# Performance work log

Hardware: AMD Instinct MI355X
Metric: run time of the kernel (lower is better)

The kernel has to match this reference:

```python
import jax, jax.numpy as jnp
import numpy as np


def _mlp(x, w1, b1, w2, b2):
    # full_connected / full_connected_conv1d with channels [3,16,32]:
    # pointwise Linear -> LeakyReLU -> Linear (kernel-size-1 conv == linear on last dim)
    h = jax.nn.leaky_relu(x @ w1 + b1)
    return h @ w2 + b2


def setup_inputs() -> dict:
    key = jax.random.key(0)
    ks = jax.random.split(key, 10)
    P, K = 100000, 16            # points, neighbors per point
    C_IN, C_H, C_OUT, C_W = 3, 16, 32, 64
    center = jax.random.normal(ks[0], (P, 1, C_IN), dtype=jnp.float32)
    other = jax.random.normal(ks[1], (P, K, C_IN), dtype=jnp.float32)
    s1 = 1.0 / np.sqrt(C_IN)
    s2 = 1.0 / np.sqrt(C_H)
    # 6 stacked 3->16->32 MLPs: [q, center_k, center_v, other_k, other_v, pos]
    mlp_w1 = jax.random.normal(ks[2], (6, C_IN, C_H), dtype=jnp.float32) * s1
    mlp_b1 = jax.random.normal(ks[3], (6, C_H), dtype=jnp.float32) * s1
    mlp_w2 = jax.random.normal(ks[4], (6, C_H, C_OUT), dtype=jnp.float32) * s2
    mlp_b2 = jax.random.normal(ks[5], (6, C_OUT), dtype=jnp.float32) * s2
    # weight_process: 32->64->32
    wp_w1 = jax.random.normal(ks[6], (C_OUT, C_W), dtype=jnp.float32) / np.sqrt(C_OUT)
    wp_b1 = jax.random.normal(ks[7], (C_W,), dtype=jnp.float32) / np.sqrt(C_OUT)
    wp_w2 = jax.random.normal(ks[8], (C_W, C_OUT), dtype=jnp.float32) / np.sqrt(C_W)
    wp_b2 = jax.random.normal(ks[9], (C_OUT,), dtype=jnp.float32) / np.sqrt(C_W)
    return {"center": center, "other": other,
            "mlp_w1": mlp_w1, "mlp_b1": mlp_b1, "mlp_w2": mlp_w2, "mlp_b2": mlp_b2,
            "wp_w1": wp_w1, "wp_b1": wp_b1, "wp_w2": wp_w2, "wp_b2": wp_b2}


def reference(center, other, mlp_w1, mlp_b1, mlp_w2, mlp_b2, wp_w1, wp_b1, wp_w2, wp_b2):
    # center: [P,1,3], other: [P,K,3]
    q = _mlp(center, mlp_w1[0], mlp_b1[0], mlp_w2[0], mlp_b2[0])      # [P,1,32]
    ck = _mlp(center, mlp_w1[1], mlp_b1[1], mlp_w2[1], mlp_b2[1])     # [P,1,32]
    cv = _mlp(center, mlp_w1[2], mlp_b1[2], mlp_w2[2], mlp_b2[2])     # [P,1,32]
    ok = _mlp(other, mlp_w1[3], mlp_b1[3], mlp_w2[3], mlp_b2[3])      # [P,K,32]
    ov = _mlp(other, mlp_w1[4], mlp_b1[4], mlp_w2[4], mlp_b2[4])      # [P,K,32]
    k_all = jnp.concatenate([ck, ok], axis=-2)                        # [P,K+1,32]
    v_all = jnp.concatenate([cv, ov], axis=-2)                        # [P,K+1,32]
    fea_minus = center - jnp.concatenate([center, other], axis=-2)    # [P,K+1,3]
    pos = _mlp(fea_minus, mlp_w1[5], mlp_b1[5], mlp_w2[5], mlp_b2[5]) # [P,K+1,32]
    fea_weight = _mlp(q - k_all + pos, wp_w1, wp_b1, wp_w2, wp_b2)    # [P,K+1,32]
    # vector attention: softmax over CHANNEL dim (-1), weighted sum over neighbors (-2)
    attn = jax.nn.softmax(fea_weight, axis=-1) * (v_all + pos)
    return jnp.sum(attn, axis=-2)                                     # [P,32]
```

## Files before the change

### kernel.cpp

```cpp
#include <hip/hip_runtime.h>


constexpr int PPB = 15;
constexpr float LOG2E = 1.44269504088896340736f;

typedef __attribute__((ext_vector_type(8))) short bf8;
typedef __attribute__((ext_vector_type(4))) float f4;

__device__ __forceinline__ float lrelu(float v) { return fmaxf(v, 0.01f * v); }

__device__ __forceinline__ unsigned int pkbf(float a, float b) {
#if __has_builtin(__builtin_amdgcn_cvt_pk_bf16_f32)
  typedef __attribute__((ext_vector_type(2))) __bf16 bf16x2;
  const bf16x2 r = __builtin_amdgcn_cvt_pk_bf16_f32(a, b);
  return __builtin_bit_cast(unsigned int, r);
#else
  const unsigned int ua = __builtin_bit_cast(unsigned int, a) + 0x8000u;
  const unsigned int ub = __builtin_bit_cast(unsigned int, b) + 0x8000u;
  return __builtin_amdgcn_perm(ub, ua, 0x07060302u);
#endif
}
__device__ __forceinline__ unsigned short us16(float a) {
  return (unsigned short)((__builtin_bit_cast(unsigned int, a) + 0x8000u) >> 16);
}
__device__ __forceinline__ bf8 mkbf8(const f4& a, const f4& b) {
  uint4 u;
  u.x = pkbf(a[0], a[1]); u.y = pkbf(a[2], a[3]);
  u.z = pkbf(b[0], b[1]); u.w = pkbf(b[2], b[3]);
  return __builtin_bit_cast(bf8, u);
}
__device__ __forceinline__ float exp2fast(float x) {
#if __has_builtin(__builtin_amdgcn_exp2f)
  return __builtin_amdgcn_exp2f(x);
#else
  float r; asm("v_exp_f32 %0, %1" : "=v"(r) : "v"(x)); return r;
#endif
}
__device__ __forceinline__ f4 mfma32(bf8 a, bf8 b, f4 c) {
  return __builtin_amdgcn_mfma_f32_16x16x32_bf16(a, b, c, 0, 0, 0);
}

__device__ __forceinline__ int slotk(int q, int j) {
  return (j < 4) ? (q * 4 + j) : (16 + q * 4 + (j - 4));
}

__device__ __forceinline__ float w1v(const float* mw1, const float* mb1,
                                     int s, int k, int n) {
  const int cb = n >> 4, cc = n & 15;
  const int sk = s ? 1 : 3, sv = s ? 2 : 4;
  if (k < 3)  return cb == 0 ? mw1[sk * 48 + k * 16 + cc]
                   : (cb == 1 ? mw1[sv * 48 + k * 16 + cc] : 0.f);
  if (k < 6)  return cb == 2 ? mw1[5 * 48 + (k - 3) * 16 + cc] : 0.f;
  if (k < 9)  return cb == 3 ? mw1[0 * 48 + (k - 6) * 16 + cc] : 0.f;
  if (k == 9) {
    const int m = (cb == 0) ? sk : (cb == 1) ? sv : (cb == 2) ? 5 : 0;
    return mb1[m * 16 + cc];
  }
  return 0.f;
}
__device__ __forceinline__ float w2v(const float* mw2, int s, int k, int n) {
  const int sk = s ? 1 : 3, sv = s ? 2 : 4;
  if (n < 32) {
    if (k < 16)            return -mw2[sk * 512 + k * 32 + n];
    if (k >= 32 && k < 48) return  mw2[5 * 512 + (k - 32) * 32 + n];
    if (k >= 48)           return  mw2[0 * 512 + (k - 48) * 32 + n];
    return 0.f;
  } else {
    const int cc = n - 32;
    if (k >= 16 && k < 32) return mw2[sv * 512 + (k - 16) * 32 + cc];
    if (k >= 32 && k < 48) return mw2[5 * 512 + (k - 32) * 32 + cc];
    return 0.f;
  }
}

__global__ void prep_kernel(const float* __restrict__ mw1, const float* __restrict__ mb1,
                            const float* __restrict__ mw2, const float* __restrict__ mb2,
                            const float* __restrict__ ww1, const float* __restrict__ ww2,
                            unsigned short* __restrict__ ws16, float* __restrict__ wsf) {
  const int tid = blockIdx.x * 256 + threadIdx.x;
  const int lane = tid & 63, q = lane >> 4, l = lane & 15;
  if (tid < 2048) {
    const int f = tid >> 6;
    for (int j = 0; j < 8; j++) {
      float v;
      if (f < 8) {
        const int s = f >> 2, c = f & 3;
        v = w1v(mw1, mb1, s, q * 8 + j, c * 16 + l);
      } else if (f < 24) {
        const int g = f - 8, s = g >> 3, mc = (g >> 1) & 3, kc2 = g & 1;
        v = w2v(mw2, s, kc2 * 32 + slotk(q, j), mc * 16 + l);
      } else if (f < 28) {
        const int mc = f - 24;
        v = ww1[slotk(q, j) * 64 + mc * 16 + l];
      } else {
        const int g = f - 28, mc2 = g >> 1, kc2 = g & 1;
        v = ww2[(kc2 * 32 + slotk(q, j)) * 32 + mc2 * 16 + l] * LOG2E;
      }
      ws16[f * 512 + lane * 8 + j] = us16(v);
    }
  } else if (tid < 2176) {
    const int t2 = tid - 2048, grp = t2 >> 5, cc = t2 & 31;
    float v;
    if (grp == 0)      v = mb2[cc] - mb2[96 + cc] + mb2[160 + cc];
    else if (grp == 1) v = mb2[128 + cc] + mb2[160 + cc];
    else if (grp == 2) v = mb2[cc] - mb2[32 + cc] + mb2[160 + cc];
    else               v = mb2[64 + cc] + mb2[160 + cc];
    wsf[grp * 32 + cc] = v;
  }
}

__global__ __launch_bounds__(256, 2) void point_attn_kernel(
    const float* __restrict__ center, const float* __restrict__ other,
    const float* __restrict__ wb1, const float* __restrict__ wb2,
    const unsigned short* __restrict__ ws16, const float* __restrict__ wsf,
    float* __restrict__ out, int P) {
  __shared__ float pr[256 * 36];
  __shared__ uint4 bf_s[4][64][2];

  const int t = threadIdx.x, lane = t & 63, wv = t >> 6;
  const int q = lane >> 4, l = lane & 15;

  {
    const int isC = (t >= 240);
    const int pt = isC ? (t - 240) : (t >> 4);
    int p = blockIdx.x * PPB + pt;
    p = p < P ? p : P - 1;
    const float c0 = center[(size_t)p * 3 + 0];
    const float c1 = center[(size_t)p * 3 + 1];
    const float c2 = center[(size_t)p * 3 + 2];
    const float* op = other + ((size_t)p * 16 + (t & 15)) * 3;
    const float o0 = op[0], o1 = op[1], o2 = op[2];
    const float x0 = isC ? c0 : o0, x1 = isC ? c1 : o1, x2 = isC ? c2 : o2;
    const float g0 = c0 - x0, g1 = c1 - x1, g2 = c2 - x2;
    uint4 s0v, s1v;
    s0v.x = pkbf(x0, x1); s0v.y = pkbf(x2, g0);
    s0v.z = pkbf(g1, g2); s0v.w = pkbf(c0, c1);
    s1v.x = pkbf(c2, 1.0f); s1v.y = 0u; s1v.z = 0u; s1v.w = 0u;
    bf_s[wv][lane][0] = s0v;
    bf_s[wv][lane][1] = s1v;
  }

  bf8 W1[4], W2[4][2], P1[4], P2[2][2];
  f4 bw[2], bvp[2], b1f[4], b2f[2];

  auto loadSet = [&](int s) {
#pragma unroll
    for (int c = 0; c < 4; c++)
      W1[c] = *(const bf8*)(ws16 + ((s * 4 + c) * 512 + lane * 8));
#pragma unroll
    for (int mc = 0; mc < 4; mc++)
#pragma unroll
      for (int kc2 = 0; kc2 < 2; kc2++)
        W2[mc][kc2] = *(const bf8*)(ws16 + ((8 + s * 8 + mc * 2 + kc2) * 512 + lane * 8));
#pragma unroll
    for (int mc = 0; mc < 2; mc++) {
      bw[mc]  = *(const f4*)(wsf + s * 64 + mc * 16 + q * 4);
      bvp[mc] = *(const f4*)(wsf + s * 64 + 32 + mc * 16 + q * 4);
    }
  };

  loadSet(wv == 3 ? 1 : 0);
#pragma unroll
  for (int mc = 0; mc < 4; mc++)
    P1[mc] = *(const bf8*)(ws16 + ((24 + mc) * 512 + lane * 8));
#pragma unroll
  for (int mc2 = 0; mc2 < 2; mc2++)
#pragma unroll
    for (int kc2 = 0; kc2 < 2; kc2++)
      P2[mc2][kc2] = *(const bf8*)(ws16 + ((28 + mc2 * 2 + kc2) * 512 + lane * 8));
#pragma unroll
  for (int mc = 0; mc < 4; mc++) b1f[mc] = *(const f4*)(wb1 + mc * 16 + q * 4);
#pragma unroll
  for (int mc2 = 0; mc2 < 2; mc2++) {
    const f4 b = *(const f4*)(wb2 + mc2 * 16 + q * 4);
#pragma unroll
    for (int j = 0; j < 4; j++) b2f[mc2][j] = b[j] * LOG2E;
  }

  auto computeTile = [&](int T) {
    const int lr = ((T & 3) << 4) | l;
    uint4 bu = {0u, 0u, 0u, 0u};
    if (q < 2) bu = bf_s[wv][lr][q];
    const bf8 bx = __builtin_bit_cast(bf8, bu);
    const f4 fzero = {0.f, 0.f, 0.f, 0.f};

    f4 D1[4];
#pragma unroll
    for (int c = 0; c < 4; c++) {
      f4 D = mfma32(W1[c], bx, fzero);
#pragma unroll
      for (int j = 0; j < 4; j++) D1[c][j] = lrelu(D[j]);
    }
    const bf8 hlo = mkbf8(D1[0], D1[1]);
    const bf8 hhi = mkbf8(D1[2], D1[3]);

    f4 wq[2], vpv[2];
#pragma unroll
    for (int mc = 0; mc < 4; mc++) {
      f4 acc = (mc < 2) ? bw[mc] : bvp[mc - 2];
      acc = mfma32(W2[mc][0], hlo, acc);
      acc = mfma32(W2[mc][1], hhi, acc);
      if (mc < 2) wq[mc] = acc; else vpv[mc - 2] = acc;
    }
    const bf8 wB = mkbf8(wq[0], wq[1]);

    f4 h2[4];
#pragma unroll
    for (int mc = 0; mc < 4; mc++) {
      f4 acc = mfma32(P1[mc], wB, b1f[mc]);
#pragma unroll
      for (int j = 0; j < 4; j++) h2[mc][j] = lrelu(acc[j]);
    }
    const bf8 h2lo = mkbf8(h2[0], h2[1]);
    const bf8 h2hi = mkbf8(h2[2], h2[3]);

    f4 fw[2];
#pragma unroll
    for (int mc2 = 0; mc2 < 2; mc2++) {
      f4 acc = mfma32(P2[mc2][0], h2lo, b2f[mc2]);
      fw[mc2] = mfma32(P2[mc2][1], h2hi, acc);
    }

    float ex[2][4], sum = 0.f;
#pragma unroll
    for (int mc = 0; mc < 2; mc++)
#pragma unroll
      for (int j = 0; j < 4; j++) {
        ex[mc][j] = exp2fast(fw[mc][j]);
        sum += ex[mc][j];
      }
    sum += __shfl_xor(sum, 16);
    sum += __shfl_xor(sum, 32);
    const float inv = __builtin_amdgcn_rcpf(sum);

    f4 p0, p1;
#pragma unroll
    for (int j = 0; j < 4; j++) {
      p0[j] = ex[0][j] * inv * vpv[0][j];
      p1[j] = ex[1][j] * inv * vpv[1][j];
    }
    *(f4*)&pr[(T * 16 + l) * 36 + q * 4] = p0;
    *(f4*)&pr[(T * 16 + l) * 36 + 16 + q * 4] = p1;
  };

  computeTile(wv == 3 ? 15 : wv * 4);
  if (wv == 3) loadSet(0);
#pragma unroll
  for (int jj = 1; jj < 4; jj++)
    computeTile(wv == 3 ? (11 + jj) : (wv * 4 + jj));

  __syncthreads();

  for (int u = t; u < 480; u += 256) {
    const int pp = u >> 5, c = u & 31;
    float s = pr[(240 + pp) * 36 + c];
#pragma unroll
    for (int r2 = 0; r2 < 16; r2++) s += pr[(pp * 16 + r2) * 36 + c];
    const int gp = blockIdx.x * PPB + pp;
    if (gp < P) out[(size_t)gp * 32 + c] = s;
  }
}

extern "C" void kernel_launch(void* const* d_in, const int* in_sizes, int n_in,
                              void* d_out, int out_size, void* d_ws, size_t ws_size,
                              hipStream_t stream) {
  const float* center = (const float*)d_in[0];
  const float* other  = (const float*)d_in[1];
  unsigned short* ws16 = (unsigned short*)d_ws;
  float* wsf = (float*)((char*)d_ws + 32768);

  prep_kernel<<<9, 256, 0, stream>>>(
      (const float*)d_in[2], (const float*)d_in[3],
      (const float*)d_in[4], (const float*)d_in[5],
      (const float*)d_in[6], (const float*)d_in[8], ws16, wsf);

  const int P = in_sizes[0] / 3;
  const int blocks = (P + PPB - 1) / PPB;
  point_attn_kernel<<<blocks, 256, 0, stream>>>(
      center, other,
      (const float*)d_in[7], (const float*)d_in[9],
      ws16, wsf, (float*)d_out, P);
}
```

Before: 142.1 us.

## Raise occupancy by streaming MLP weights and storing partial results as bf16

Launch bounds go from 2 to 4 blocks per CU, and the per-wave cached W1/W2 weight fragments are gone. Each tile now reloads those weights from global memory (likely cache hits), which frees registers to fit the higher occupancy. The shared buffer of per-neighbor weighted values is now packed as bf16 pairs, roughly halving LDS use. The final neighbor reduction reads packed pairs and writes float2 outputs. The costs are more weight-load traffic per tile and extra precision loss from rounding intermediate products to bf16 before summing.

```diff
diff --git a/kernel.cpp b/kernel.cpp
--- a/kernel.cpp
+++ b/kernel.cpp
@@ -28,6 +28,12 @@
   u.x = pkbf(a[0], a[1]); u.y = pkbf(a[2], a[3]);
   u.z = pkbf(b[0], b[1]); u.w = pkbf(b[2], b[3]);
   return __builtin_bit_cast(bf8, u);
+}
+__device__ __forceinline__ float bf2f_lo(unsigned int u) {
+  return __builtin_bit_cast(float, u << 16);
+}
+__device__ __forceinline__ float bf2f_hi(unsigned int u) {
+  return __builtin_bit_cast(float, u & 0xffff0000u);
 }
 __device__ __forceinline__ float exp2fast(float x) {
 #if __has_builtin(__builtin_amdgcn_exp2f)
@@ -109,12 +115,12 @@
   }
 }
 
-__global__ __launch_bounds__(256, 2) void point_attn_kernel(
+__global__ __launch_bounds__(256, 4) void point_attn_kernel(
     const float* __restrict__ center, const float* __restrict__ other,
     const float* __restrict__ wb1, const float* __restrict__ wb2,
     const unsigned short* __restrict__ ws16, const float* __restrict__ wsf,
     float* __restrict__ out, int P) {
-  __shared__ float pr[256 * 36];
+  __shared__ unsigned int pr[256 * 20];
   __shared__ uint4 bf_s[4][64][2];
 
   const int t = threadIdx.x, lane = t & 63, wv = t >> 6;
@@ -140,18 +146,10 @@
     bf_s[wv][lane][1] = s1v;
   }
 
-  bf8 W1[4], W2[4][2], P1[4], P2[2][2];
+  bf8 P1[4], P2[2][2];
   f4 bw[2], bvp[2], b1f[4], b2f[2];
 
-  auto loadSet = [&](int s) {
-#pragma unroll
-    for (int c = 0; c < 4; c++)
-      W1[c] = *(const bf8*)(ws16 + ((s * 4 + c) * 512 + lane * 8));
-#pragma unroll
-    for (int mc = 0; mc < 4; mc++)
-#pragma unroll
-      for (int kc2 = 0; kc2 < 2; kc2++)
-        W2[mc][kc2] = *(const bf8*)(ws16 + ((8 + s * 8 + mc * 2 + kc2) * 512 + lane * 8));
+  auto biasSet = [&](int s) {
 #pragma unroll
     for (int mc = 0; mc < 2; mc++) {
       bw[mc]  = *(const f4*)(wsf + s * 64 + mc * 16 + q * 4);
@@ -159,7 +157,7 @@
     }
   };
 
-  loadSet(wv == 3 ? 1 : 0);
+  biasSet(wv == 3 ? 1 : 0);
 #pragma unroll
   for (int mc = 0; mc < 4; mc++)
     P1[mc] = *(const bf8*)(ws16 + ((24 + mc) * 512 + lane * 8));
@@ -177,7 +175,7 @@
     for (int j = 0; j < 4; j++) b2f[mc2][j] = b[j] * LOG2E;
   }
 
-  auto computeTile = [&](int T) {
+  auto computeTile = [&](int T, int s) {
     const int lr = ((T & 3) << 4) | l;
     uint4 bu = {0u, 0u, 0u, 0u};
     if (q < 2) bu = bf_s[wv][lr][q];
@@ -187,7 +185,8 @@
     f4 D1[4];
 #pragma unroll
     for (int c = 0; c < 4; c++) {
-      f4 D = mfma32(W1[c], bx, fzero);
+      const bf8 W1c = *(const bf8*)(ws16 + ((s * 4 + c) * 512 + lane * 8));
+      f4 D = mfma32(W1c, bx, fzero);
 #pragma unroll
       for (int j = 0; j < 4; j++) D1[c][j] = lrelu(D[j]);
     }
@@ -197,9 +196,11 @@
     f4 wq[2], vpv[2];
 #pragma unroll
     for (int mc = 0; mc < 4; mc++) {
+      const bf8 W2a = *(const bf8*)(ws16 + ((8 + s * 8 + mc * 2 + 0) * 512 + lane * 8));
+      const bf8 W2b = *(const bf8*)(ws16 + ((8 + s * 8 + mc * 2 + 1) * 512 + lane * 8));
       f4 acc = (mc < 2) ? bw[mc] : bvp[mc - 2];
-      acc = mfma32(W2[mc][0], hlo, acc);
-      acc = mfma32(W2[mc][1], hhi, acc);
+      acc = mfma32(W2a, hlo, acc);
+      acc = mfma32(W2b, hhi, acc);
       if (mc < 2) wq[mc] = acc; else vpv[mc - 2] = acc;
     }
     const bf8 wB = mkbf8(wq[0], wq[1]);
@@ -239,25 +240,39 @@
       p0[j] = ex[0][j] * inv * vpv[0][j];
       p1[j] = ex[1][j] * inv * vpv[1][j];
     }
-    *(f4*)&pr[(T * 16 + l) * 36 + q * 4] = p0;
-    *(f4*)&pr[(T * 16 + l) * 36 + 16 + q * 4] = p1;
+    const int row = T * 16 + l;
+    uint2 u0, u1;
+    u0.x = pkbf(p0[0], p0[1]); u0.y = pkbf(p0[2], p0[3]);
+    u1.x = pkbf(p1[0], p1[1]); u1.y = pkbf(p1[2], p1[3]);
+    *(uint2*)&pr[row * 20 + 2 * q] = u0;
+    *(uint2*)&pr[row * 20 + 8 + 2 * q] = u1;
   };
 
-  computeTile(wv == 3 ? 15 : wv * 4);
-  if (wv == 3) loadSet(0);
-#pragma unroll
-  for (int jj = 1; jj < 4; jj++)
-    computeTile(wv == 3 ? (11 + jj) : (wv * 4 + jj));
+  if (wv == 3) {
+    computeTile(15, 1);
+    biasSet(0);
+    computeTile(12, 0); computeTile(13, 0); computeTile(14, 0);
+  } else {
+#pragma unroll
+    for (int jj = 0; jj < 4; jj++) computeTile(wv * 4 + jj, 0);
+  }
 
   __syncthreads();
 
-  for (int u = t; u < 480; u += 256) {
-    const int pp = u >> 5, c = u & 31;
-    float s = pr[(240 + pp) * 36 + c];
-#pragma unroll
-    for (int r2 = 0; r2 < 16; r2++) s += pr[(pp * 16 + r2) * 36 + c];
+  if (t < 240) {
+    const int pp = t >> 4, i = t & 15;
+    unsigned int u = pr[(240 + pp) * 20 + i];
+    float slo = bf2f_lo(u), shi = bf2f_hi(u);
+#pragma unroll
+    for (int r2 = 0; r2 < 16; r2++) {
+      u = pr[(pp * 16 + r2) * 20 + i];
+      slo += bf2f_lo(u); shi += bf2f_hi(u);
+    }
     const int gp = blockIdx.x * PPB + pp;
-    if (gp < P) out[(size_t)gp * 32 + c] = s;
+    if (gp < P) {
+      float2 o; o.x = slo; o.y = shi;
+      *(float2*)(out + (size_t)gp * 32 + i * 2) = o;
+    }
   }
 }
 
```

Result: slower. 196.3 us (+38.1%).
